# Kernel optimization log

Hardware: AMD Instinct MI355X
Metric: run time of the kernel (lower is better)

The kernel has to match this reference:

```python
import jax, jax.numpy as jnp
import numpy as np

N_FEATURES = 26          # number of feature categories (FEATURE_AND_ENCODER entries)
VOCAB_PER_FEATURE = 50000  # ids in [f*V, (f+1)*V) belong to feature f
SLOTS_PER_FEATURE = 8
BATCH = 16384
EMBED = 32
VOCAB = N_FEATURES * VOCAB_PER_FEATURE


def setup_inputs() -> dict:
    key = jax.random.key(0)
    ks = jax.random.split(key, 8)
    P = N_FEATURES * SLOTS_PER_FEATURE  # 208 ids per row
    x = jax.random.randint(ks[0], (BATCH, P), 0, VOCAB, dtype=jnp.int64)
    table = jax.random.normal(ks[1], (VOCAB, EMBED), dtype=jnp.float32) * 0.1
    D = N_FEATURES * EMBED  # 832
    W0 = jax.random.normal(ks[2], (D, 64), dtype=jnp.float32) * (1.0 / np.sqrt(D))
    b0 = jax.random.normal(ks[3], (64,), dtype=jnp.float32) * 0.01
    W1 = jax.random.normal(ks[4], (64, 16), dtype=jnp.float32) * (1.0 / 8.0)
    b1 = jax.random.normal(ks[5], (16,), dtype=jnp.float32) * 0.01
    W2 = jax.random.normal(ks[6], (16, 1), dtype=jnp.float32) * 0.25
    return {"x": x, "table": table, "W0": W0, "b0": b0, "W1": W1, "b1": b1, "W2": W2}


def reference(x, table, W0, b0, W1, b1, W2):
    B = x.shape[0]
    # dynamic embedding lookup: [B, P, E]
    embeds = table[x]
    # category of each id (what encoder.match_category encodes): [B, P]
    cat = x // VOCAB_PER_FEATURE
    # mask+gather+reduce_sum per feature == one-hot segment sum over features
    onehot = jax.nn.one_hot(cat, N_FEATURES, dtype=table.dtype)  # [B, P, F]
    pooled = jnp.einsum('bpe,bpf->bfe', embeds, onehot)          # [B, F, E]
    feats = pooled.reshape(B, N_FEATURES * EMBED)                # concat of per-feature sums
    h = jax.nn.relu(feats @ W0 + b0)
    h = jax.nn.relu(h @ W1 + b1)
    logits = h @ W2
    return jax.nn.sigmoid(logits)
```

## Files before the change

kernel.cpp:

```cpp
#include <hip/hip_runtime.h>
#include <math.h>

#define BATCH 16384
#define PP    208
#define NF    26
#define VPF   50000u
#define EMB   32
#define DD    832
#define VOCAB (NF * 50000)

typedef __attribute__((ext_vector_type(8))) short short8v;
typedef __attribute__((ext_vector_type(4))) float float4v;

static __device__ __forceinline__ ushort f32_to_bf16(float f) {
    unsigned u = __builtin_bit_cast(unsigned, f);
    unsigned r = (u + 0x7fffu + ((u >> 16) & 1u)) >> 16;
    return (ushort)r;
}
static __device__ __forceinline__ unsigned pack_bf16x2(float lo, float hi) {
    return (unsigned)f32_to_bf16(lo) | ((unsigned)f32_to_bf16(hi) << 16);
}

__global__ __launch_bounds__(256) void prep_tbl(const float* __restrict__ table,
                                                ushort* __restrict__ tbl16) {
    const size_t i = ((size_t)blockIdx.x * 256 + threadIdx.x) * 8;
    if (i >= (size_t)VOCAB * EMB) return;
    const float4 a = *reinterpret_cast<const float4*>(table + i);
    const float4 b = *reinterpret_cast<const float4*>(table + i + 4);
    uint4 o;
    o.x = pack_bf16x2(a.x, a.y);
    o.y = pack_bf16x2(a.z, a.w);
    o.z = pack_bf16x2(b.x, b.y);
    o.w = pack_bf16x2(b.z, b.w);
    *reinterpret_cast<uint4*>(tbl16 + i) = o;
}

__global__ __launch_bounds__(256) void prep_w0(const float* __restrict__ W0,
                                               ushort* __restrict__ w0p) {
    const int i = blockIdx.x * 256 + threadIdx.x;
    if (i < DD * 64) {
        const int k = i >> 6, c = i & 63;
        const int kt = k >> 5, kk = k & 31;
        w0p[(kt * 64 + c) * 32 + kk] = f32_to_bf16(W0[i]);
    }
}

__global__ __launch_bounds__(256, 4) void pool_kernel(const int* __restrict__ x,
                                                      const ushort* __restrict__ tbl,
                                                      ushort* __restrict__ feats) {
    __shared__ int   s_ids[PP];
    __shared__ float s_pool[DD];

    const int    tid = threadIdx.x;
    const size_t row = blockIdx.x;

    for (int i = tid; i < DD; i += 256) s_pool[i] = 0.0f;
    if (tid < PP / 4)
        reinterpret_cast<int4*>(s_ids)[tid] =
            reinterpret_cast<const int4*>(x + row * PP)[tid];
    __syncthreads();

    const int g = tid >> 4;
    const int l = tid & 15;

    unsigned ids[13];
#pragma unroll
    for (int p = 0; p < 13; ++p) ids[p] = (unsigned)s_ids[p * 16 + g];

    unsigned vals[13];
#pragma unroll
    for (int p = 0; p < 13; ++p)
        vals[p] = *reinterpret_cast<const unsigned*>(tbl + (size_t)ids[p] * EMB + 2 * l);

    float* pool = s_pool + 2 * l;
#pragma unroll
    for (int p = 0; p < 13; ++p) {
        const unsigned cat = ids[p] / VPF;
        const float f0 = __builtin_bit_cast(float, vals[p] << 16);
        const float f1 = __builtin_bit_cast(float, vals[p] & 0xffff0000u);
        atomicAdd(pool + cat * EMB + 0, f0);
        atomicAdd(pool + cat * EMB + 1, f1);
    }
    __syncthreads();

    if (tid < DD / 4) {
        ushort4 o;
        o.x = f32_to_bf16(s_pool[tid * 4 + 0]);
        o.y = f32_to_bf16(s_pool[tid * 4 + 1]);
        o.z = f32_to_bf16(s_pool[tid * 4 + 2]);
        o.w = f32_to_bf16(s_pool[tid * 4 + 3]);
        *reinterpret_cast<ushort4*>(feats + row * DD + tid * 4) = o;
    }
}

__global__ __launch_bounds__(256, 4) void pool_kernel_f32(const int* __restrict__ x,
                                                          const float* __restrict__ table,
                                                          ushort* __restrict__ feats) {
    __shared__ int   s_ids[PP];
    __shared__ float s_pool[DD];

    const int    tid = threadIdx.x;
    const size_t row = blockIdx.x;

    for (int i = tid; i < DD; i += 256) s_pool[i] = 0.0f;
    if (tid < PP / 4)
        reinterpret_cast<int4*>(s_ids)[tid] =
            reinterpret_cast<const int4*>(x + row * PP)[tid];
    __syncthreads();

    const int e  = tid & 31;
    const int p0 = (tid >> 5) * 26;
    float* pool  = s_pool + e;

#pragma unroll 1
    for (int b = 0; b < 24; b += 4) {
        const unsigned id0 = (unsigned)s_ids[p0 + b + 0];
        const unsigned id1 = (unsigned)s_ids[p0 + b + 1];
        const unsigned id2 = (unsigned)s_ids[p0 + b + 2];
        const unsigned id3 = (unsigned)s_ids[p0 + b + 3];
        const float v0 = table[(size_t)id0 * EMB + e];
        const float v1 = table[(size_t)id1 * EMB + e];
        const float v2 = table[(size_t)id2 * EMB + e];
        const float v3 = table[(size_t)id3 * EMB + e];
        atomicAdd(pool + (id0 / VPF) * EMB, v0);
        atomicAdd(pool + (id1 / VPF) * EMB, v1);
        atomicAdd(pool + (id2 / VPF) * EMB, v2);
        atomicAdd(pool + (id3 / VPF) * EMB, v3);
    }
    {
        const unsigned idA = (unsigned)s_ids[p0 + 24];
        const unsigned idB = (unsigned)s_ids[p0 + 25];
        const float vA = table[(size_t)idA * EMB + e];
        const float vB = table[(size_t)idB * EMB + e];
        atomicAdd(pool + (idA / VPF) * EMB, vA);
        atomicAdd(pool + (idB / VPF) * EMB, vB);
    }
    __syncthreads();

    if (tid < DD / 4) {
        ushort4 o;
        o.x = f32_to_bf16(s_pool[tid * 4 + 0]);
        o.y = f32_to_bf16(s_pool[tid * 4 + 1]);
        o.z = f32_to_bf16(s_pool[tid * 4 + 2]);
        o.w = f32_to_bf16(s_pool[tid * 4 + 3]);
        *reinterpret_cast<ushort4*>(feats + row * DD + tid * 4) = o;
    }
}

__global__ __launch_bounds__(128) void mlp_kernel(const ushort* __restrict__ feats,
                                                  const ushort* __restrict__ w0p,
                                                  const float* __restrict__ b0,
                                                  const float* __restrict__ W1,
                                                  const float* __restrict__ b1,
                                                  const float* __restrict__ W2,
                                                  float* __restrict__ out) {
    __shared__ float sC[16][68];
    __shared__ float sH1[16][17];
    __shared__ float sB0[64];

    const int tid   = threadIdx.x;
    const int wid   = tid >> 6;
    const int lane  = tid & 63;
    const int lrow  = lane & 15;
    const int lk    = lane >> 4;
    const int brow0 = blockIdx.x * 16;

    if (tid < 64) sB0[tid] = b0[tid];

    float4v acc[4];
#pragma unroll
    for (int n = 0; n < 4; ++n) acc[n] = (float4v){0.f, 0.f, 0.f, 0.f};

    const int kt0 = wid * 13;
    const ushort* frow  = feats + (size_t)(brow0 + lrow) * DD + lk * 8;
    const ushort* wbase = w0p + lrow * 32 + lk * 8;

    short8v a_cur, a_nxt;
    short8v b_cur[4], b_nxt[4];
    a_cur = *reinterpret_cast<const short8v*>(frow + kt0 * 32);
#pragma unroll
    for (int n = 0; n < 4; ++n)
        b_cur[n] = *reinterpret_cast<const short8v*>(wbase + (size_t)(kt0 * 64 + n * 16) * 32);

#pragma unroll
    for (int i = 0; i < 13; ++i) {
        if (i < 12) {
            const int kt = kt0 + i + 1;
            a_nxt = *reinterpret_cast<const short8v*>(frow + kt * 32);
#pragma unroll
            for (int n = 0; n < 4; ++n)
                b_nxt[n] = *reinterpret_cast<const short8v*>(wbase + (size_t)(kt * 64 + n * 16) * 32);
        }
#pragma unroll
        for (int n = 0; n < 4; ++n)
            acc[n] = __builtin_amdgcn_mfma_f32_16x16x32_bf16(a_cur, b_cur[n], acc[n], 0, 0, 0);
        a_cur = a_nxt;
#pragma unroll
        for (int n = 0; n < 4; ++n) b_cur[n] = b_nxt[n];
    }

    if (wid == 0) {
#pragma unroll
        for (int n = 0; n < 4; ++n)
#pragma unroll
            for (int r = 0; r < 4; ++r)
                sC[lk * 4 + r][n * 16 + lrow] = acc[n][r];
    }
    __syncthreads();
    if (wid == 1) {
#pragma unroll
        for (int n = 0; n < 4; ++n)
#pragma unroll
            for (int r = 0; r < 4; ++r)
                sC[lk * 4 + r][n * 16 + lrow] += acc[n][r];
    }
    __syncthreads();

    {
        const int r = tid >> 3, c = (tid & 7) * 2;
        float a0 = b1[c], a1 = b1[c + 1];
#pragma unroll 8
        for (int k = 0; k < 64; ++k) {
            const float h = fmaxf(sC[r][k] + sB0[k], 0.f);
            const float2 wv = *reinterpret_cast<const float2*>(W1 + k * 16 + c);
            a0 = fmaf(h, wv.x, a0);
            a1 = fmaf(h, wv.y, a1);
        }
        sH1[r][c + 0] = fmaxf(a0, 0.f);
        sH1[r][c + 1] = fmaxf(a1, 0.f);
    }
    __syncthreads();

    if (tid < 16) {
        float z = 0.f;
#pragma unroll
        for (int j = 0; j < 16; ++j) z = fmaf(sH1[tid][j], W2[j], z);
        out[brow0 + tid] = 1.f / (1.f + expf(-z));
    }
}

extern "C" void kernel_launch(void* const* d_in, const int* in_sizes, int n_in,
                              void* d_out, int out_size, void* d_ws, size_t ws_size,
                              hipStream_t stream) {
    const int*   x     = (const int*)d_in[0];
    const float* table = (const float*)d_in[1];
    const float* W0    = (const float*)d_in[2];
    const float* b0    = (const float*)d_in[3];
    const float* W1    = (const float*)d_in[4];
    const float* b1    = (const float*)d_in[5];
    const float* W2    = (const float*)d_in[6];
    float*       out   = (float*)d_out;

    ushort* feats16 = (ushort*)d_ws;
    ushort* w0p     = feats16 + (size_t)BATCH * DD;
    ushort* tbl16   = w0p + (size_t)DD * 64;
    const size_t need = ((size_t)BATCH * DD + (size_t)DD * 64 + (size_t)VOCAB * EMB) * 2;

    prep_w0<<<(DD * 64 + 255) / 256, 256, 0, stream>>>(W0, w0p);

    if (ws_size >= need) {
        const int nconv = ((int)((size_t)VOCAB * EMB / 8) + 255) / 256;
        prep_tbl<<<nconv, 256, 0, stream>>>(table, tbl16);
        pool_kernel<<<BATCH, 256, 0, stream>>>(x, tbl16, feats16);
    } else {
        pool_kernel_f32<<<BATCH, 256, 0, stream>>>(x, table, feats16);
    }

    mlp_kernel<<<BATCH / 16, 128, 0, stream>>>(feats16, w0p, b0, W1, b1, W2, out);
}
```

Before: 815.5 us.

## Bucket-sort ids per row and sweep table in address order for locality

Adds a per-row counting sort of ids into 80 address buckets, then a pooling kernel that processes 8 rows per block, walking the buckets in order so that table gathers run roughly in ascending address order and get better cache and TLB locality. The MLP is restructured to 4 waves that each own 16 output columns over the full K range, which drops the cross-wave reduction through shared memory. The f32 fallback loop is simplified. This costs an extra kernel pass plus workspace traffic for the sorted ids and offsets, and the sweep loop is serial and branchy per thread.

```diff
diff --git a/kernel.cpp b/kernel.cpp
--- a/kernel.cpp
+++ b/kernel.cpp
@@ -8,6 +8,9 @@
 #define EMB   32
 #define DD    832
 #define VOCAB (NF * 50000)
+
+#define SLSH  14
+#define NS    80
 
 typedef __attribute__((ext_vector_type(8))) short short8v;
 typedef __attribute__((ext_vector_type(4))) float float4v;
@@ -45,9 +48,95 @@
     }
 }
 
-__global__ __launch_bounds__(256, 4) void pool_kernel(const int* __restrict__ x,
-                                                      const ushort* __restrict__ tbl,
-                                                      ushort* __restrict__ feats) {
+__global__ __launch_bounds__(256) void sort_prep(const int* __restrict__ x,
+                                                 int* __restrict__ sorted,
+                                                 ushort* __restrict__ offs) {
+    __shared__ int s_id[PP];
+    __shared__ int s_cnt[NS];
+    __shared__ int s_base[NS + 1];
+
+    const int    tid = threadIdx.x;
+    const size_t row = blockIdx.x;
+
+    if (tid < PP / 4)
+        reinterpret_cast<int4*>(s_id)[tid] =
+            reinterpret_cast<const int4*>(x + row * PP)[tid];
+    if (tid < NS) s_cnt[tid] = 0;
+    __syncthreads();
+
+    if (tid < PP) atomicAdd(&s_cnt[((unsigned)s_id[tid]) >> SLSH], 1);
+    __syncthreads();
+
+    if (tid == 0) {
+        int acc = 0;
+        for (int s = 0; s < NS; ++s) { s_base[s] = acc; acc += s_cnt[s]; }
+        s_base[NS] = acc;
+    }
+    __syncthreads();
+
+    if (tid < NS) s_cnt[tid] = s_base[tid];
+    if (tid <= NS) offs[row * (NS + 1) + tid] = (ushort)s_base[tid];
+    __syncthreads();
+
+    if (tid < PP) {
+        const int id  = s_id[tid];
+        const int pos = atomicAdd(&s_cnt[((unsigned)id) >> SLSH], 1);
+        sorted[row * PP + pos] = id;
+    }
+}
+
+__global__ __launch_bounds__(256) void pool_sweep(const int* __restrict__ sorted,
+                                                  const ushort* __restrict__ offs,
+                                                  const ushort* __restrict__ tbl,
+                                                  ushort* __restrict__ feats) {
+    __shared__ float  s_pool[8 * DD];
+    __shared__ ushort s_off[8 * (NS + 1)];
+
+    const int tid  = threadIdx.x;
+    const int row0 = blockIdx.x * 8;
+
+    for (int i = tid; i < 8 * DD; i += 256) s_pool[i] = 0.0f;
+    for (int i = tid; i < 8 * (NS + 1); i += 256) {
+        const int r = i / (NS + 1), s = i - r * (NS + 1);
+        s_off[i] = offs[(size_t)(row0 + r) * (NS + 1) + s];
+    }
+    __syncthreads();
+
+    const int g = tid >> 4;
+    const int l = tid & 15;
+    const int r = g >> 1;
+    const int h = g & 1;
+
+    const ushort* offr = s_off + r * (NS + 1);
+    float*        pool = s_pool + r * DD + 2 * l;
+    const int*    srow = sorted + (size_t)(row0 + r) * PP;
+
+    for (int s = 0; s < NS; ++s) {
+        const int e = offr[s + 1];
+        for (int j = offr[s] + h; j < e; j += 2) {
+            const unsigned id = (unsigned)srow[j];
+            const unsigned v  = *reinterpret_cast<const unsigned*>(
+                                    tbl + (size_t)id * EMB + 2 * l);
+            const unsigned cat = id / VPF;
+            atomicAdd(pool + cat * EMB + 0, __builtin_bit_cast(float, v << 16));
+            atomicAdd(pool + cat * EMB + 1, __builtin_bit_cast(float, v & 0xffff0000u));
+        }
+    }
+    __syncthreads();
+
+    for (int i = tid; i < 8 * DD / 4; i += 256) {
+        ushort4 o;
+        o.x = f32_to_bf16(s_pool[i * 4 + 0]);
+        o.y = f32_to_bf16(s_pool[i * 4 + 1]);
+        o.z = f32_to_bf16(s_pool[i * 4 + 2]);
+        o.w = f32_to_bf16(s_pool[i * 4 + 3]);
+        *reinterpret_cast<ushort4*>(feats + (size_t)row0 * DD + i * 4) = o;
+    }
+}
+
+__global__ __launch_bounds__(256, 4) void pool_bf16(const int* __restrict__ x,
+                                                    const ushort* __restrict__ tbl,
+                                                    ushort* __restrict__ feats) {
     __shared__ int   s_ids[PP];
     __shared__ float s_pool[DD];
 
@@ -66,7 +155,6 @@
     unsigned ids[13];
 #pragma unroll
     for (int p = 0; p < 13; ++p) ids[p] = (unsigned)s_ids[p * 16 + g];
-
     unsigned vals[13];
 #pragma unroll
     for (int p = 0; p < 13; ++p)
@@ -76,10 +164,8 @@
 #pragma unroll
     for (int p = 0; p < 13; ++p) {
         const unsigned cat = ids[p] / VPF;
-        const float f0 = __builtin_bit_cast(float, vals[p] << 16);
-        const float f1 = __builtin_bit_cast(float, vals[p] & 0xffff0000u);
-        atomicAdd(pool + cat * EMB + 0, f0);
-        atomicAdd(pool + cat * EMB + 1, f1);
+        atomicAdd(pool + cat * EMB + 0, __builtin_bit_cast(float, vals[p] << 16));
+        atomicAdd(pool + cat * EMB + 1, __builtin_bit_cast(float, vals[p] & 0xffff0000u));
     }
     __syncthreads();
 
@@ -93,9 +179,9 @@
     }
 }
 
-__global__ __launch_bounds__(256, 4) void pool_kernel_f32(const int* __restrict__ x,
-                                                          const float* __restrict__ table,
-                                                          ushort* __restrict__ feats) {
+__global__ __launch_bounds__(256, 4) void pool_f32(const int* __restrict__ x,
+                                                   const float* __restrict__ table,
+                                                   ushort* __restrict__ feats) {
     __shared__ int   s_ids[PP];
     __shared__ float s_pool[DD];
 
@@ -113,27 +199,13 @@
     float* pool  = s_pool + e;
 
 #pragma unroll 1
-    for (int b = 0; b < 24; b += 4) {
+    for (int b = 0; b < 26; b += 2) {
         const unsigned id0 = (unsigned)s_ids[p0 + b + 0];
         const unsigned id1 = (unsigned)s_ids[p0 + b + 1];
-        const unsigned id2 = (unsigned)s_ids[p0 + b + 2];
-        const unsigned id3 = (unsigned)s_ids[p0 + b + 3];
         const float v0 = table[(size_t)id0 * EMB + e];
         const float v1 = table[(size_t)id1 * EMB + e];
-        const float v2 = table[(size_t)id2 * EMB + e];
-        const float v3 = table[(size_t)id3 * EMB + e];
         atomicAdd(pool + (id0 / VPF) * EMB, v0);
         atomicAdd(pool + (id1 / VPF) * EMB, v1);
-        atomicAdd(pool + (id2 / VPF) * EMB, v2);
-        atomicAdd(pool + (id3 / VPF) * EMB, v3);
-    }
-    {
-        const unsigned idA = (unsigned)s_ids[p0 + 24];
-        const unsigned idB = (unsigned)s_ids[p0 + 25];
-        const float vA = table[(size_t)idA * EMB + e];
-        const float vB = table[(size_t)idB * EMB + e];
-        atomicAdd(pool + (idA / VPF) * EMB, vA);
-        atomicAdd(pool + (idB / VPF) * EMB, vB);
     }
     __syncthreads();
 
@@ -147,87 +219,51 @@
     }
 }
 
-__global__ __launch_bounds__(128) void mlp_kernel(const ushort* __restrict__ feats,
+__global__ __launch_bounds__(256) void mlp_kernel(const ushort* __restrict__ feats,
                                                   const ushort* __restrict__ w0p,
                                                   const float* __restrict__ b0,
                                                   const float* __restrict__ W1,
                                                   const float* __restrict__ b1,
                                                   const float* __restrict__ W2,
                                                   float* __restrict__ out) {
-    __shared__ float sC[16][68];
+    __shared__ float sH[16][65];
     __shared__ float sH1[16][17];
-    __shared__ float sB0[64];
 
     const int tid   = threadIdx.x;
-    const int wid   = tid >> 6;
+    const int w     = tid >> 6;
     const int lane  = tid & 63;
     const int lrow  = lane & 15;
     const int lk    = lane >> 4;
     const int brow0 = blockIdx.x * 16;
 
-    if (tid < 64) sB0[tid] = b0[tid];
-
-    float4v acc[4];
-#pragma unroll
-    for (int n = 0; n < 4; ++n) acc[n] = (float4v){0.f, 0.f, 0.f, 0.f};
-
-    const int kt0 = wid * 13;
+    float4v acc = (float4v){0.f, 0.f, 0.f, 0.f};
+
     const ushort* frow  = feats + (size_t)(brow0 + lrow) * DD + lk * 8;
-    const ushort* wbase = w0p + lrow * 32 + lk * 8;
-
-    short8v a_cur, a_nxt;
-    short8v b_cur[4], b_nxt[4];
-    a_cur = *reinterpret_cast<const short8v*>(frow + kt0 * 32);
-#pragma unroll
-    for (int n = 0; n < 4; ++n)
-        b_cur[n] = *reinterpret_cast<const short8v*>(wbase + (size_t)(kt0 * 64 + n * 16) * 32);
-
-#pragma unroll
-    for (int i = 0; i < 13; ++i) {
-        if (i < 12) {
-            const int kt = kt0 + i + 1;
-            a_nxt = *reinterpret_cast<const short8v*>(frow + kt * 32);
-#pragma unroll
-            for (int n = 0; n < 4; ++n)
-                b_nxt[n] = *reinterpret_cast<const short8v*>(wbase + (size_t)(kt * 64 + n * 16) * 32);
-        }
-#pragma unroll
-        for (int n = 0; n < 4; ++n)
-            acc[n] = __builtin_amdgcn_mfma_f32_16x16x32_bf16(a_cur, b_cur[n], acc[n], 0, 0, 0);
-        a_cur = a_nxt;
-#pragma unroll
-        for (int n = 0; n < 4; ++n) b_cur[n] = b_nxt[n];
-    }
-
-    if (wid == 0) {
-#pragma unroll
-        for (int n = 0; n < 4; ++n)
-#pragma unroll
-            for (int r = 0; r < 4; ++r)
-                sC[lk * 4 + r][n * 16 + lrow] = acc[n][r];
-    }
-    __syncthreads();
-    if (wid == 1) {
-#pragma unroll
-        for (int n = 0; n < 4; ++n)
-#pragma unroll
-            for (int r = 0; r < 4; ++r)
-                sC[lk * 4 + r][n * 16 + lrow] += acc[n][r];
-    }
-    __syncthreads();
+    const ushort* wbase = w0p + (size_t)(w * 16 + lrow) * 32 + lk * 8;
+
+#pragma unroll 2
+    for (int kt = 0; kt < 26; ++kt) {
+        const short8v a = *reinterpret_cast<const short8v*>(frow + kt * 32);
+        const short8v b = *reinterpret_cast<const short8v*>(wbase + (size_t)kt * 64 * 32);
+        acc = __builtin_amdgcn_mfma_f32_16x16x32_bf16(a, b, acc, 0, 0, 0);
+    }
 
     {
-        const int r = tid >> 3, c = (tid & 7) * 2;
-        float a0 = b1[c], a1 = b1[c + 1];
+        const int   col = w * 16 + lrow;
+        const float bb  = b0[col];
+#pragma unroll
+        for (int r = 0; r < 4; ++r)
+            sH[lk * 4 + r][col] = fmaxf(acc[r] + bb, 0.f);
+    }
+    __syncthreads();
+
+    {
+        const int r = tid >> 4, c = tid & 15;
+        float a0 = b1[c];
 #pragma unroll 8
-        for (int k = 0; k < 64; ++k) {
-            const float h = fmaxf(sC[r][k] + sB0[k], 0.f);
-            const float2 wv = *reinterpret_cast<const float2*>(W1 + k * 16 + c);
-            a0 = fmaf(h, wv.x, a0);
-            a1 = fmaf(h, wv.y, a1);
-        }
-        sH1[r][c + 0] = fmaxf(a0, 0.f);
-        sH1[r][c + 1] = fmaxf(a1, 0.f);
+        for (int k = 0; k < 64; ++k)
+            a0 = fmaf(sH[r][k], W1[k * 16 + c], a0);
+        sH1[r][c] = fmaxf(a0, 0.f);
     }
     __syncthreads();
 
@@ -254,17 +290,26 @@
     ushort* feats16 = (ushort*)d_ws;
     ushort* w0p     = feats16 + (size_t)BATCH * DD;
     ushort* tbl16   = w0p + (size_t)DD * 64;
-    const size_t need = ((size_t)BATCH * DD + (size_t)DD * 64 + (size_t)VOCAB * EMB) * 2;
+    int*    sorted  = (int*)(tbl16 + (size_t)VOCAB * EMB);
+    ushort* offs    = (ushort*)(sorted + (size_t)BATCH * PP);
+
+    const size_t need_t2 = ((size_t)BATCH * DD + (size_t)DD * 64 + (size_t)VOCAB * EMB) * 2;
+    const size_t need_t1 = need_t2 + (size_t)BATCH * PP * 4 + (size_t)BATCH * (NS + 1) * 2;
 
     prep_w0<<<(DD * 64 + 255) / 256, 256, 0, stream>>>(W0, w0p);
 
-    if (ws_size >= need) {
+    if (ws_size >= need_t1) {
         const int nconv = ((int)((size_t)VOCAB * EMB / 8) + 255) / 256;
         prep_tbl<<<nconv, 256, 0, stream>>>(table, tbl16);
-        pool_kernel<<<BATCH, 256, 0, stream>>>(x, tbl16, feats16);
+        sort_prep<<<BATCH, 256, 0, stream>>>(x, sorted, offs);
+        pool_sweep<<<BATCH / 8, 256, 0, stream>>>(sorted, offs, tbl16, feats16);
+    } else if (ws_size >= need_t2) {
+        const int nconv = ((int)((size_t)VOCAB * EMB / 8) + 255) / 256;
+        prep_tbl<<<nconv, 256, 0, stream>>>(table, tbl16);
+        pool_bf16<<<BATCH, 256, 0, stream>>>(x, tbl16, feats16);
     } else {
-        pool_kernel_f32<<<BATCH, 256, 0, stream>>>(x, table, feats16);
-    }
-
-    mlp_kernel<<<BATCH / 16, 128, 0, stream>>>(feats16, w0p, b0, W1, b1, W2, out);
-}
+        pool_f32<<<BATCH, 256, 0, stream>>>(x, table, feats16);
+    }
+
+    mlp_kernel<<<BATCH / 16, 256, 0, stream>>>(feats16, w0p, b0, W1, b1, W2, out);
+}
```

New measurement: 851.1 us. +4.4%, slower.
